# Optimization experiments

Measured on AMD Instinct MI355X. Metric: run time of the kernel, lower is better.

The kernel has to match this reference:

```python
import jax, jax.numpy as jnp
import numpy as np

B, S, D, E, K, F = 2, 1024, 1024, 8, 2, 2048


def setup_inputs() -> dict:
    key = jax.random.key(0)
    k0, k1, k2, k3 = jax.random.split(key, 4)
    x = jax.random.normal(k0, (B, S, D), dtype=jnp.float32)
    gate_w = (jax.random.normal(k1, (E, D), dtype=jnp.float32) * 0.02)  # nn.init.normal_(std=0.02)
    # nn.Linear default init ~ U(-1/sqrt(fan_in), 1/sqrt(fan_in)); use same scale
    w1 = jax.random.uniform(k2, (E, F, D), dtype=jnp.float32, minval=-1.0, maxval=1.0) / np.float32(np.sqrt(D))
    w2 = jax.random.uniform(k3, (E, D, F), dtype=jnp.float32, minval=-1.0, maxval=1.0) / np.float32(np.sqrt(F))
    norm_w = jnp.ones((D,), dtype=jnp.float32)
    scale = jnp.full((1,), -4.0, dtype=jnp.float32)
    return {"x": x, "gate_w": gate_w, "w1": w1, "w2": w2, "norm_w": norm_w, "scale": scale}


def reference(x, gate_w, w1, w2, norm_w, scale):
    b, s, d = x.shape
    e = gate_w.shape[0]
    t = b * s
    eps = jnp.finfo(x.dtype).eps  # torch RMSNorm eps=None -> dtype eps
    # RMSNorm
    xn = x * jax.lax.rsqrt(jnp.mean(x * x, axis=-1, keepdims=True) + eps) * norm_w
    xf = xn.reshape(t, d)
    # router
    logits = xf @ gate_w.T                       # [T, E]
    prob = jax.nn.softmax(logits, axis=-1)
    topk_w, topk_e = jax.lax.top_k(prob, K)      # [T, K]
    topk_w = topk_w / jnp.clip(jnp.sum(topk_w, axis=-1, keepdims=True), 1e-6)
    # dense combine weights [T, E]: sum of slot weights routed to each expert
    combine = jnp.sum(jax.nn.one_hot(topk_e, e, dtype=xf.dtype) * topk_w[..., None], axis=1)
    # all-expert FFN, weighted combine (same math as the gather/index_add loop)
    h = jax.nn.silu(jnp.einsum('td,efd->tef', xf, w1))   # [T, E, F]
    out = jnp.einsum('tef,edf,te->td', h, w2, combine)    # [T, D]
    # load-balance aux loss (Switch eq.4), f_e from top-1 slot, detached
    f_e = jnp.mean(jax.nn.one_hot(topk_e[:, 0], e, dtype=prob.dtype), axis=0)
    lb_loss = e * jnp.sum(jax.lax.stop_gradient(f_e) * jnp.mean(prob, axis=0))
    sc = jax.nn.sigmoid(scale)[0]
    return (x + sc * out.reshape(b, s, d), lb_loss)
```

## Files before the change

### kernel.cpp

```cpp
#include <hip/hip_runtime.h>
#include <stdint.h>

#define T_TOK 2048
#define DD 1024
#define EE 8
#define FF 2048
#define NSLOT 4096
#define SLOTPAD 4224

typedef __attribute__((ext_vector_type(8))) __bf16 bf16x8;
typedef __attribute__((ext_vector_type(4))) float floatx4;
typedef __attribute__((ext_vector_type(8))) unsigned short ushort8;

__device__ __forceinline__ unsigned short f2bf(float f){
  union { float f; unsigned u; } v; v.f = f;
  unsigned r = v.u + 0x7fffu + ((v.u >> 16) & 1u);
  return (unsigned short)(r >> 16);
}
__device__ __forceinline__ float bf2f(unsigned short h){
  union { unsigned u; float f; } v; v.u = (unsigned)h << 16; return v.f;
}

#define GLDS(src, dst) __builtin_amdgcn_global_load_lds( \
    (__attribute__((address_space(1))) unsigned int*)(src), \
    (__attribute__((address_space(3))) unsigned int*)(dst), 16, 0, 0)

__global__ __launch_bounds__(256) void k_rms_router(
    const float* __restrict__ x, const float* __restrict__ gw,
    const float* __restrict__ nw,
    unsigned short* __restrict__ xn,
    int* __restrict__ topk_id, float* __restrict__ topk_w,
    float* __restrict__ probbuf)
{
  const int t = blockIdx.x, tid = threadIdx.x;
  const float4 xv = ((const float4*)(x + (size_t)t * DD))[tid];
  float ss = xv.x*xv.x + xv.y*xv.y + xv.z*xv.z + xv.w*xv.w;
  #pragma unroll
  for (int o = 32; o > 0; o >>= 1) ss += __shfl_down(ss, o);
  __shared__ float s_ss[4];
  __shared__ float s_p[4][8];
  if ((tid & 63) == 0) s_ss[tid >> 6] = ss;
  __syncthreads();
  const float tot = s_ss[0] + s_ss[1] + s_ss[2] + s_ss[3];
  const float inv = rsqrtf(tot * (1.0f / DD) + 1.1920929e-7f);
  const float4 nv = ((const float4*)nw)[tid];
  float4 xnv;
  xnv.x = xv.x*inv*nv.x; xnv.y = xv.y*inv*nv.y;
  xnv.z = xv.z*inv*nv.z; xnv.w = xv.w*inv*nv.w;
  ushort4 bv; bv.x = f2bf(xnv.x); bv.y = f2bf(xnv.y); bv.z = f2bf(xnv.z); bv.w = f2bf(xnv.w);
  ((ushort4*)(xn + (size_t)t * DD))[tid] = bv;
  float p[8];
  #pragma unroll
  for (int e = 0; e < 8; e++){
    const float4 g = ((const float4*)(gw + e * DD))[tid];
    p[e] = xnv.x*g.x + xnv.y*g.y + xnv.z*g.z + xnv.w*g.w;
  }
  #pragma unroll
  for (int e = 0; e < 8; e++){
    #pragma unroll
    for (int o = 32; o > 0; o >>= 1) p[e] += __shfl_down(p[e], o);
  }
  if ((tid & 63) == 0){
    #pragma unroll
    for (int e = 0; e < 8; e++) s_p[tid >> 6][e] = p[e];
  }
  __syncthreads();
  if (tid == 0){
    float lg[8], pr[8];
    #pragma unroll
    for (int e = 0; e < 8; e++) lg[e] = s_p[0][e] + s_p[1][e] + s_p[2][e] + s_p[3][e];
    float mx = lg[0];
    for (int e = 1; e < 8; e++) mx = fmaxf(mx, lg[e]);
    float sum = 0.f;
    for (int e = 0; e < 8; e++){ pr[e] = __expf(lg[e] - mx); sum += pr[e]; }
    const float is = 1.f / sum;
    for (int e = 0; e < 8; e++) pr[e] *= is;
    #pragma unroll
    for (int e = 0; e < 8; e++) probbuf[t * 8 + e] = pr[e];
    int e1 = 0;
    for (int e = 1; e < 8; e++) if (pr[e] > pr[e1]) e1 = e;
    int e2 = (e1 == 0) ? 1 : 0;
    for (int e = 0; e < 8; e++) if (e != e1 && e != e2 && pr[e] > pr[e2]) e2 = e;
    const float wsum = fmaxf(pr[e1] + pr[e2], 1e-6f);
    topk_id[2*t] = e1; topk_id[2*t+1] = e2;
    topk_w[2*t] = pr[e1] / wsum; topk_w[2*t+1] = pr[e2] / wsum;
  }
}

__global__ __launch_bounds__(256) void k_stats(
    const int* __restrict__ topk_id, const float* __restrict__ topk_w,
    const float* __restrict__ probbuf,
    int* __restrict__ counts, int* __restrict__ bases,
    int* __restrict__ slots_of, int* __restrict__ tok_of,
    float* __restrict__ slot_w,
    float* __restrict__ lb_out)
{
  const int tid = threadIdx.x;
  __shared__ int s_scan[256][8];
  __shared__ int s_base[8];

  int ids[16];
  int lc[8] = {}, lc1[8] = {};
  float lsp[8] = {};
  #pragma unroll
  for (int j = 0; j < 8; j++){
    const int t = tid * 8 + j;
    const int e1 = topk_id[2*t], e2 = topk_id[2*t+1];
    ids[2*j] = e1; ids[2*j+1] = e2;
    lc[e1]++; lc[e2]++; lc1[e1]++;
    const float4 p0 = ((const float4*)(probbuf + t * 8))[0];
    const float4 p1 = ((const float4*)(probbuf + t * 8))[1];
    lsp[0] += p0.x; lsp[1] += p0.y; lsp[2] += p0.z; lsp[3] += p0.w;
    lsp[4] += p1.x; lsp[5] += p1.y; lsp[6] += p1.z; lsp[7] += p1.w;
  }
  #pragma unroll
  for (int e = 0; e < 8; e++) s_scan[tid][e] = lc[e];
  __syncthreads();
  for (int off = 1; off < 256; off <<= 1){
    int v[8];
    if (tid >= off){
      #pragma unroll
      for (int e = 0; e < 8; e++) v[e] = s_scan[tid - off][e];
    }
    __syncthreads();
    if (tid >= off){
      #pragma unroll
      for (int e = 0; e < 8; e++) s_scan[tid][e] += v[e];
    }
    __syncthreads();
  }
  int   rc1[8]; float rsp[8];
  #pragma unroll
  for (int e = 0; e < 8; e++){ rc1[e] = lc1[e]; rsp[e] = lsp[e]; }
  #pragma unroll
  for (int e = 0; e < 8; e++){
    #pragma unroll
    for (int o = 32; o > 0; o >>= 1){
      rc1[e] += __shfl_down(rc1[e], o);
      rsp[e] += __shfl_down(rsp[e], o);
    }
  }
  __shared__ int   s_c1[4][8];
  __shared__ float s_sp[4][8];
  if ((tid & 63) == 0){
    const int w = tid >> 6;
    #pragma unroll
    for (int e = 0; e < 8; e++){ s_c1[w][e] = rc1[e]; s_sp[w][e] = rsp[e]; }
  }
  __syncthreads();
  if (tid == 0){
    int b = 0; float lb = 0.f;
    for (int e = 0; e < 8; e++){
      const int tot = s_scan[255][e];
      counts[e] = tot; bases[e] = b; s_base[e] = b; b += tot;
      const int   c1 = s_c1[0][e] + s_c1[1][e] + s_c1[2][e] + s_c1[3][e];
      const float sp = s_sp[0][e] + s_sp[1][e] + s_sp[2][e] + s_sp[3][e];
      lb += (float)c1 * sp;
    }
    lb_out[0] = 8.f * lb * (1.f / ((float)T_TOK * (float)T_TOK));
  }
  __syncthreads();
  int rank[8];
  #pragma unroll
  for (int e = 0; e < 8; e++) rank[e] = s_scan[tid][e] - lc[e];
  #pragma unroll
  for (int j = 0; j < 8; j++){
    const int t = tid * 8 + j;
    #pragma unroll
    for (int k = 0; k < 2; k++){
      const int e = ids[2*j + k];
      const int slot = s_base[e] + rank[e]++;
      slots_of[2*t + k] = slot;
      tok_of[slot] = t;
      slot_w[slot] = topk_w[2*t + k];
    }
  }
}

template<int KD, int NDIM, int MODE>
__global__ __launch_bounds__(256) void k_gemm(
    const unsigned short* __restrict__ Ag,
    const float* __restrict__ Bw,
    const int* __restrict__ counts, const int* __restrict__ bases,
    const int* __restrict__ tok_of,
    unsigned short* __restrict__ Cout)
{
  const int e = blockIdx.x & 7;
  const int g = blockIdx.x >> 3;
  int nt, ms, kbase; size_t poff;
  if (MODE == 0){ nt = g & 31; ms = g >> 5; kbase = 0; poff = 0; }
  else { const int ks = g & 1; nt = (g >> 1) & 15; ms = g >> 5; kbase = ks * 1024;
         poff = (size_t)ks * SLOTPAD * NDIM; }
  const int M = counts[e];
  if (M == 0) return;
  const int sbase = bases[e];

  __shared__ __align__(16) unsigned short As[2][128 * 32];
  __shared__ __align__(16) unsigned short Bs[2][64 * 32];

  const int tid = threadIdx.x;
  const int l = tid & 63;
  const int w = tid >> 6;
  const int wm = (w >> 1) * 64, wn = (w & 1) * 32;
  const int lrow = l & 15, lq = l >> 4;

  const int ar0 = tid >> 2, ar1 = (tid + 256) >> 2, aq = tid & 3;
  const int akc0 = ((aq - (ar0 >> 1)) & 3) * 8;
  const int akc1 = ((aq - (ar1 >> 1)) & 3) * 8;
  const int br = tid >> 2, bq = tid & 3;
  const int bkc = ((bq - (br >> 1)) & 3) * 8;

  const float* brow = Bw + (size_t)e * NDIM * KD + (size_t)(nt * 64 + br) * KD + kbase + bkc;

  for (int mt = ms; mt * 128 < M; mt += 4){
    const unsigned short *arow0, *arow1;
    {
      const int v0 = min(mt * 128 + ar0, M - 1);
      const int v1 = min(mt * 128 + ar1, M - 1);
      const int r0 = (MODE == 0) ? tok_of[sbase + v0] : (sbase + v0);
      const int r1 = (MODE == 0) ? tok_of[sbase + v1] : (sbase + v1);
      arow0 = Ag + (size_t)r0 * KD + kbase + akc0;
      arow1 = Ag + (size_t)r1 * KD + kbase + akc1;
    }

    floatx4 acc[4][2] = {};

    GLDS(arow0, As[0] + tid * 8);
    GLDS(arow1, As[0] + (tid + 256) * 8);
    {
      const float4 b0 = ((const float4*)brow)[0], b1 = ((const float4*)brow)[1];
      ushort8 o;
      o[0]=f2bf(b0.x); o[1]=f2bf(b0.y); o[2]=f2bf(b0.z); o[3]=f2bf(b0.w);
      o[4]=f2bf(b1.x); o[5]=f2bf(b1.y); o[6]=f2bf(b1.z); o[7]=f2bf(b1.w);
      *(ushort8*)(Bs[0] + tid * 8) = o;
    }

    for (int kk = 0; kk < 32; kk++){
      const int cur = kk & 1, nxt = cur ^ 1;
      __syncthreads();
      const bool more = (kk < 31);
      float4 b0, b1;
      if (more){
        const int ko = (kk + 1) * 32;
        GLDS(arow0 + ko, As[nxt] + tid * 8);
        GLDS(arow1 + ko, As[nxt] + (tid + 256) * 8);
        b0 = ((const float4*)(brow + ko))[0];
        b1 = ((const float4*)(brow + ko))[1];
      }
      bf16x8 af[4], bfv[2];
      #pragma unroll
      for (int mi = 0; mi < 4; mi++){
        const int row = wm + mi * 16 + lrow;
        const int p = (lq + (row >> 1)) & 3;
        af[mi] = *(const bf16x8*)(As[cur] + row * 32 + p * 8);
      }
      #pragma unroll
      for (int ni = 0; ni < 2; ni++){
        const int row = wn + ni * 16 + lrow;
        const int p = (lq + (row >> 1)) & 3;
        bfv[ni] = *(const bf16x8*)(Bs[cur] + row * 32 + p * 8);
      }
      #pragma unroll
      for (int mi = 0; mi < 4; mi++)
        #pragma unroll
        for (int ni = 0; ni < 2; ni++)
          acc[mi][ni] = __builtin_amdgcn_mfma_f32_16x16x32_bf16(af[mi], bfv[ni], acc[mi][ni], 0, 0, 0);
      if (more){
        ushort8 o;
        o[0]=f2bf(b0.x); o[1]=f2bf(b0.y); o[2]=f2bf(b0.z); o[3]=f2bf(b0.w);
        o[4]=f2bf(b1.x); o[5]=f2bf(b1.y); o[6]=f2bf(b1.z); o[7]=f2bf(b1.w);
        *(ushort8*)(Bs[nxt] + tid * 8) = o;
      }
    }

    const int rb = lq * 4;
    #pragma unroll
    for (int mi = 0; mi < 4; mi++){
      #pragma unroll
      for (int r = 0; r < 4; r++){
        const int row = mt * 128 + wm + mi * 16 + rb + r;
        if (row < M){
          #pragma unroll
          for (int ni = 0; ni < 2; ni++){
            const int col = nt * 64 + wn + ni * 16 + (l & 15);
            const float v = acc[mi][ni][r];
            if (MODE == 0){
              const float s = v / (1.f + __expf(-v));
              Cout[(size_t)(sbase + row) * NDIM + col] = f2bf(s);
            } else {
              Cout[poff + (size_t)(sbase + row) * NDIM + col] = f2bf(v);
            }
          }
        }
      }
    }
    __syncthreads();
  }
}

__global__ __launch_bounds__(256) void k_combine(
    const float* __restrict__ x, const unsigned short* __restrict__ Og,
    const int* __restrict__ slots_of, const float* __restrict__ slot_w,
    const float* __restrict__ scale,
    float* __restrict__ out)
{
  const int i = blockIdx.x * 256 + threadIdx.x;
  const int t = i >> 7;
  const int j = i & 127;
  const int s0 = slots_of[2*t], s1 = slots_of[2*t+1];
  const float w0 = slot_w[s0], w1 = slot_w[s1];
  const ushort8 a0 = ((const ushort8*)(Og + (size_t)s0 * DD))[j];
  const ushort8 a1 = ((const ushort8*)(Og + (size_t)SLOTPAD * DD + (size_t)s0 * DD))[j];
  const ushort8 b0 = ((const ushort8*)(Og + (size_t)s1 * DD))[j];
  const ushort8 b1 = ((const ushort8*)(Og + (size_t)SLOTPAD * DD + (size_t)s1 * DD))[j];
  const float4 x0 = ((const float4*)(x + (size_t)t * DD))[2*j];
  const float4 x1 = ((const float4*)(x + (size_t)t * DD))[2*j + 1];
  const float sc = 1.f / (1.f + __expf(-scale[0]));
  float o[8];
  #pragma unroll
  for (int q = 0; q < 8; q++)
    o[q] = sc * (w0 * (bf2f(a0[q]) + bf2f(a1[q])) + w1 * (bf2f(b0[q]) + bf2f(b1[q])));
  float4 o0, o1;
  o0.x = x0.x + o[0]; o0.y = x0.y + o[1]; o0.z = x0.z + o[2]; o0.w = x0.w + o[3];
  o1.x = x1.x + o[4]; o1.y = x1.y + o[5]; o1.z = x1.z + o[6]; o1.w = x1.w + o[7];
  ((float4*)(out + (size_t)t * DD))[2*j] = o0;
  ((float4*)(out + (size_t)t * DD))[2*j + 1] = o1;
}

extern "C" void kernel_launch(void* const* d_in, const int* in_sizes, int n_in,
                              void* d_out, int out_size, void* d_ws, size_t ws_size,
                              hipStream_t stream)
{
  const float* x     = (const float*)d_in[0];
  const float* gw    = (const float*)d_in[1];
  const float* w1    = (const float*)d_in[2];
  const float* w2    = (const float*)d_in[3];
  const float* nw    = (const float*)d_in[4];
  const float* scale = (const float*)d_in[5];
  float* out = (float*)d_out;

  char* ws = (char*)d_ws;
  int*   counts  = (int*)(ws + 0);
  int*   bases   = (int*)(ws + 64);
  int*   topk_id = (int*)(ws + 1024);
  float* topk_w  = (float*)(ws + 20480);
  int*   slots_of= (int*)(ws + 40960);
  float* slot_w  = (float*)(ws + 61440);
  int*   tok_of  = (int*)(ws + 81920);
  float* probbuf = (float*)(ws + 102400);
  unsigned short* xn  = (unsigned short*)(ws + 262144);
  unsigned short* Hg  = xn + (size_t)T_TOK * DD;
  unsigned short* Og  = Hg + (size_t)SLOTPAD * FF;

  k_rms_router<<<T_TOK, 256, 0, stream>>>(x, gw, nw, xn, topk_id, topk_w, probbuf);
  k_stats<<<1, 256, 0, stream>>>(topk_id, topk_w, probbuf, counts, bases,
                                 slots_of, tok_of, slot_w, out + (size_t)T_TOK * DD);
  k_gemm<1024, 2048, 0><<<EE * 4 * 32, 256, 0, stream>>>(xn, w1, counts, bases, tok_of, Hg);
  k_gemm<2048, 1024, 1><<<EE * 4 * 16 * 2, 256, 0, stream>>>(Hg, w2, counts, bases, nullptr, Og);
  k_combine<<<T_TOK * DD / 8 / 256, 256, 0, stream>>>(x, Og, slots_of, slot_w, scale, out);
}
```

Before: 268.1 us.

## Pre-convert expert weights to bf16 and stream them via direct-to-LDS loads

Adds a kernel that converts w1 and w2 from fp32 to bf16 into workspace on every call. Both expert GEMMs then load B tiles with global_load_lds, the same way as A, instead of doing fp32 register loads, in-register bf16 conversion and LDS stores. The goal is to halve the weight bytes each GEMM block re-reads and to make the B-operand prefetch asynchronous. The cost is an extra full pass over the fp32 weights, bf16 writes to 64 MB of extra workspace, and the bf16 re-read in the GEMMs.

Result: slower. 279.1 us (+4.1%).

```diff
diff --git a/kernel.cpp b/kernel.cpp
--- a/kernel.cpp
+++ b/kernel.cpp
@@ -24,6 +24,21 @@
 #define GLDS(src, dst) __builtin_amdgcn_global_load_lds( \
     (__attribute__((address_space(1))) unsigned int*)(src), \
     (__attribute__((address_space(3))) unsigned int*)(dst), 16, 0, 0)
+
+__global__ __launch_bounds__(256) void k_cvt(const float* __restrict__ w1,
+    const float* __restrict__ w2, unsigned short* __restrict__ w1b,
+    unsigned short* __restrict__ w2b)
+{
+  const int n4 = EE * FF * DD / 4;
+  int i = blockIdx.x * 256 + threadIdx.x;
+  const int stride = gridDim.x * 256;
+  for (; i < 2 * n4; i += stride){
+    const int j = (i < n4) ? i : i - n4;
+    const float4 v = (i < n4) ? ((const float4*)w1)[j] : ((const float4*)w2)[j];
+    ushort4 o; o.x = f2bf(v.x); o.y = f2bf(v.y); o.z = f2bf(v.z); o.w = f2bf(v.w);
+    if (i < n4) ((ushort4*)w1b)[j] = o; else ((ushort4*)w2b)[j] = o;
+  }
+}
 
 __global__ __launch_bounds__(256) void k_rms_router(
     const float* __restrict__ x, const float* __restrict__ gw,
@@ -180,7 +195,7 @@
 template<int KD, int NDIM, int MODE>
 __global__ __launch_bounds__(256) void k_gemm(
     const unsigned short* __restrict__ Ag,
-    const float* __restrict__ Bw,
+    const unsigned short* __restrict__ Bw,
     const int* __restrict__ counts, const int* __restrict__ bases,
     const int* __restrict__ tok_of,
     unsigned short* __restrict__ Cout)
@@ -210,7 +225,8 @@
   const int br = tid >> 2, bq = tid & 3;
   const int bkc = ((bq - (br >> 1)) & 3) * 8;
 
-  const float* brow = Bw + (size_t)e * NDIM * KD + (size_t)(nt * 64 + br) * KD + kbase + bkc;
+  const unsigned short* brow =
+      Bw + (size_t)e * NDIM * KD + (size_t)(nt * 64 + br) * KD + kbase + bkc;
 
   for (int mt = ms; mt * 128 < M; mt += 4){
     const unsigned short *arow0, *arow1;
@@ -227,25 +243,16 @@
 
     GLDS(arow0, As[0] + tid * 8);
     GLDS(arow1, As[0] + (tid + 256) * 8);
-    {
-      const float4 b0 = ((const float4*)brow)[0], b1 = ((const float4*)brow)[1];
-      ushort8 o;
-      o[0]=f2bf(b0.x); o[1]=f2bf(b0.y); o[2]=f2bf(b0.z); o[3]=f2bf(b0.w);
-      o[4]=f2bf(b1.x); o[5]=f2bf(b1.y); o[6]=f2bf(b1.z); o[7]=f2bf(b1.w);
-      *(ushort8*)(Bs[0] + tid * 8) = o;
-    }
+    GLDS(brow,  Bs[0] + tid * 8);
 
     for (int kk = 0; kk < 32; kk++){
       const int cur = kk & 1, nxt = cur ^ 1;
       __syncthreads();
-      const bool more = (kk < 31);
-      float4 b0, b1;
-      if (more){
+      if (kk < 31){
         const int ko = (kk + 1) * 32;
         GLDS(arow0 + ko, As[nxt] + tid * 8);
         GLDS(arow1 + ko, As[nxt] + (tid + 256) * 8);
-        b0 = ((const float4*)(brow + ko))[0];
-        b1 = ((const float4*)(brow + ko))[1];
+        GLDS(brow + ko,  Bs[nxt] + tid * 8);
       }
       bf16x8 af[4], bfv[2];
       #pragma unroll
@@ -265,12 +272,6 @@
         #pragma unroll
         for (int ni = 0; ni < 2; ni++)
           acc[mi][ni] = __builtin_amdgcn_mfma_f32_16x16x32_bf16(af[mi], bfv[ni], acc[mi][ni], 0, 0, 0);
-      if (more){
-        ushort8 o;
-        o[0]=f2bf(b0.x); o[1]=f2bf(b0.y); o[2]=f2bf(b0.z); o[3]=f2bf(b0.w);
-        o[4]=f2bf(b1.x); o[5]=f2bf(b1.y); o[6]=f2bf(b1.z); o[7]=f2bf(b1.w);
-        *(ushort8*)(Bs[nxt] + tid * 8) = o;
-      }
     }
 
     const int rb = lq * 4;
@@ -351,11 +352,14 @@
   unsigned short* xn  = (unsigned short*)(ws + 262144);
   unsigned short* Hg  = xn + (size_t)T_TOK * DD;
   unsigned short* Og  = Hg + (size_t)SLOTPAD * FF;
-
+  unsigned short* w1b = Og + (size_t)2 * SLOTPAD * DD;
+  unsigned short* w2b = w1b + (size_t)EE * FF * DD;
+
+  k_cvt<<<2048, 256, 0, stream>>>(w1, w2, w1b, w2b);
   k_rms_router<<<T_TOK, 256, 0, stream>>>(x, gw, nw, xn, topk_id, topk_w, probbuf);
   k_stats<<<1, 256, 0, stream>>>(topk_id, topk_w, probbuf, counts, bases,
                                  slots_of, tok_of, slot_w, out + (size_t)T_TOK * DD);
-  k_gemm<1024, 2048, 0><<<EE * 4 * 32, 256, 0, stream>>>(xn, w1, counts, bases, tok_of, Hg);
-  k_gemm<2048, 1024, 1><<<EE * 4 * 16 * 2, 256, 0, stream>>>(Hg, w2, counts, bases, nullptr, Og);
+  k_gemm<1024, 2048, 0><<<EE * 4 * 32, 256, 0, stream>>>(xn, w1b, counts, bases, tok_of, Hg);
+  k_gemm<2048, 1024, 1><<<EE * 4 * 16 * 2, 256, 0, stream>>>(Hg, w2b, counts, bases, nullptr, Og);
   k_combine<<<T_TOK * DD / 8 / 256, 256, 0, stream>>>(x, Og, slots_of, slot_w, scale, out);
 }
```
